# Kernel tuning notes

Hardware: AMD Instinct MI355X
Metric: run time of the kernel (lower is better)

Reference implementation:

```python
import jax, jax.numpy as jnp
import numpy as np

D_MODEL = 1024
NUM_HEADS = 16
DEPTH = D_MODEL // NUM_HEADS


def setup_inputs() -> dict:
    key = jax.random.key(0)
    ks = jax.random.split(key, 9)
    B, S = 2, 2048
    s = 1.0 / np.sqrt(D_MODEL)
    return {
        "x": jax.random.normal(ks[0], (B, S, D_MODEL), dtype=jnp.float32),
        "wq": jax.random.normal(ks[1], (D_MODEL, D_MODEL), dtype=jnp.float32) * s,
        "bq": jnp.zeros((D_MODEL,), dtype=jnp.float32),
        "wk": jax.random.normal(ks[2], (D_MODEL, D_MODEL), dtype=jnp.float32) * s,
        "bk": jnp.zeros((D_MODEL,), dtype=jnp.float32),
        "wv": jax.random.normal(ks[3], (D_MODEL, D_MODEL), dtype=jnp.float32) * s,
        "bv": jnp.zeros((D_MODEL,), dtype=jnp.float32),
        "wo": jax.random.normal(ks[4], (D_MODEL, D_MODEL), dtype=jnp.float32) * s,
        "bo": jnp.zeros((D_MODEL,), dtype=jnp.float32),
    }


def _split_heads(t):
    # [B, S, D] -> [B, H, S, depth]
    B, S, _ = t.shape
    return t.reshape(B, S, NUM_HEADS, DEPTH).transpose(0, 2, 1, 3)


def reference(x, wq, bq, wk, bk, wv, bv, wo, bo):
    B, S, _ = x.shape
    q = _split_heads(x @ wq + bq)
    k = _split_heads(x @ wk + bk)
    v = _split_heads(x @ wv + bv)
    scale = 1.0 / jnp.sqrt(jnp.asarray(DEPTH, dtype=x.dtype))
    logits = jnp.einsum("bhsd,bhtd->bhst", q, k) * scale  # [B,H,S,S]
    attn = jax.nn.softmax(logits, axis=-1)
    ctx = jnp.einsum("bhst,bhtd->bhsd", attn, v)  # [B,H,S,depth]
    concat = ctx.transpose(0, 2, 1, 3).reshape(B, S, D_MODEL)
    return concat @ wo + bo
```

## Files before the change

### kernel.cpp

```cpp
#include <hip/hip_runtime.h>
#include <hip/hip_bf16.h>

typedef __bf16 bf16;
typedef __bf16 bf16x4 __attribute__((ext_vector_type(4)));
typedef __bf16 bf16x8 __attribute__((ext_vector_type(8)));
typedef float f32x4 __attribute__((ext_vector_type(4)));

typedef __attribute__((address_space(3))) void lds_void;
typedef const __attribute__((address_space(1))) void gbl_void;

#define D_MODEL 1024
#define NHEAD 16
#define DEPTH 64
#define SEQ 2048
#define BATCH 2
#define NTOK (BATCH * SEQ)

#define Q_SCALE 0.18033688f

__global__ __launch_bounds__(256) void prep(const float* __restrict__ w0,
                                            const float* __restrict__ w1,
                                            const float* __restrict__ w2,
                                            const float* __restrict__ w3,
                                            const float* __restrict__ x,
                                            bf16* __restrict__ wtb,
                                            bf16* __restrict__ xb) {
    int z = blockIdx.z;
    int tx = threadIdx.x, ty = threadIdx.y;
    if (z < 4) {
        const float* w = (z == 0) ? w0 : (z == 1) ? w1 : (z == 2) ? w2 : w3;
        bf16* d = wtb + (size_t)z * D_MODEL * D_MODEL;
        __shared__ float tile[32][33];
        int c0 = blockIdx.x * 32;
        int r0 = blockIdx.y * 32;
#pragma unroll
        for (int i = 0; i < 4; i++)
            tile[ty + i * 8][tx] = w[(size_t)(r0 + ty + i * 8) * D_MODEL + c0 + tx];
        __syncthreads();
#pragma unroll
        for (int i = 0; i < 4; i++)
            d[(size_t)(c0 + ty + i * 8) * D_MODEL + r0 + tx] = (bf16)tile[tx][ty + i * 8];
    } else {
        int t = ty * 32 + tx;
        size_t i = ((size_t)(z - 4) * 1024 + blockIdx.y * 32 + blockIdx.x) * 256 + t;
        float4 v = ((const float4*)x)[i];
        bf16x4 o = {(bf16)v.x, (bf16)v.y, (bf16)v.z, (bf16)v.w};
        *(bf16x4*)&xb[i * 4] = o;
    }
}

__global__ __launch_bounds__(512, 2) void qkv_gemm(const bf16* __restrict__ xb,
                                                   const bf16* __restrict__ wtb,
                                                   const float* __restrict__ bq,
                                                   const float* __restrict__ bk,
                                                   const float* __restrict__ bv,
                                                   bf16* __restrict__ q,
                                                   bf16* __restrict__ k,
                                                   bf16* __restrict__ v) {
    __shared__ bf16 sm[65536];

    const int flat = blockIdx.x;
    const int wg = (flat & 7) * 24 + (flat >> 3);
    const int mt = wg & 15, nt = wg >> 4;
    const int row0 = mt << 8;
    const int z = nt >> 2;
    const int nb = (nt & 3) << 8;

    const int tid = threadIdx.x;
    const int lane = tid & 63, wave = tid >> 6;
    const int wm = wave >> 2, wn = wave & 3;
    const int quad = lane >> 4, l16 = lane & 15;
    const int kch = ((quad ^ ((l16 >> 1) & 3)) << 3);

    const int srow = lane >> 2;
    const int scg = (lane & 3) ^ ((lane >> 3) & 3);
    const int stDst = wave * 1024 + lane * 8;

    const bf16* Ag = xb + (size_t)(row0 + wave * 32 + srow) * D_MODEL + scg * 8;
    const bf16* Bg = wtb + (size_t)z * D_MODEL * D_MODEL
                   + (size_t)(nb + wave * 32 + srow) * D_MODEL + scg * 8;

    f32x4 acc[8][4] = {};
    bf16x8 bfr[4];

#define GLL(SRC, DST) __builtin_amdgcn_global_load_lds((gbl_void*)(SRC), (lds_void*)(DST), 16, 0, 0)
#define STG_A(T_, KQ_, BUF_) { \
    const bf16* s_ = Ag + (T_) * 64 + (KQ_) * 32; \
    bf16* d_ = sm + (BUF_) * 16384 + (KQ_) * 8192 + stDst; \
    GLL(s_, d_); GLL(s_ + 16 * D_MODEL, d_ + 512); }
#define STG_B(T_, KQ_, BUF_) { \
    const bf16* s_ = Bg + (T_) * 64 + (KQ_) * 32; \
    bf16* d_ = sm + 32768 + (BUF_) * 16384 + (KQ_) * 8192 + stDst; \
    GLL(s_, d_); GLL(s_ + 16 * D_MODEL, d_ + 512); }
#define WAIT6 { asm volatile("s_waitcnt vmcnt(6)" ::: "memory"); }
#define NOW

#define PHASE(BUF_, KQ_, MQ_, STG_STMT, WAIT_STMT) { \
    bf16x8 af[4]; \
    const int ab_ = (BUF_) * 16384 + (KQ_) * 8192 + (wm * 128 + (MQ_) * 64 + l16) * 32 + kch; \
    _Pragma("unroll") \
    for (int i_ = 0; i_ < 4; i_++) af[i_] = *(const bf16x8*)&sm[ab_ + i_ * 512]; \
    if ((MQ_) == 0) { \
        const int bb_ = 32768 + (BUF_) * 16384 + (KQ_) * 8192 + (wn * 64 + l16) * 32 + kch; \
        _Pragma("unroll") \
        for (int j_ = 0; j_ < 4; j_++) bfr[j_] = *(const bf16x8*)&sm[bb_ + j_ * 512]; \
    } \
    STG_STMT; \
    WAIT_STMT; \
    __builtin_amdgcn_sched_barrier(0); \
    __builtin_amdgcn_s_barrier(); \
    __builtin_amdgcn_s_setprio(1); \
    _Pragma("unroll") \
    for (int i_ = 0; i_ < 4; i_++) \
        _Pragma("unroll") \
        for (int j_ = 0; j_ < 4; j_++) \
            acc[(MQ_) * 4 + i_][j_] = __builtin_amdgcn_mfma_f32_16x16x32_bf16( \
                af[i_], bfr[j_], acc[(MQ_) * 4 + i_][j_], 0, 0, 0); \
    __builtin_amdgcn_s_setprio(0); \
    __builtin_amdgcn_sched_barrier(0); \
    __builtin_amdgcn_s_barrier(); }

    STG_B(0, 0, 0);
    STG_A(0, 0, 0);
    STG_B(0, 1, 0);
    STG_A(0, 1, 0);
    asm volatile("s_waitcnt vmcnt(4)" ::: "memory");
    STG_B(1, 0, 1);
    STG_A(1, 0, 1);
    STG_B(1, 1, 1);
    asm volatile("s_waitcnt vmcnt(6)" ::: "memory");
    __builtin_amdgcn_sched_barrier(0);
    __builtin_amdgcn_s_barrier();

#pragma unroll 1
    for (int it = 0; it < 8; ++it) {
        const int t1 = 2 * it + 1;
        const int t2 = (2 * it + 2) & 15;
        const int t3 = (2 * it + 3) & 15;
        PHASE(0, 0, 0, STG_A(t1, 1, 1), NOW)
        PHASE(0, 0, 1, STG_B(t2, 0, 0), NOW)
        PHASE(0, 1, 0, STG_A(t2, 0, 0), NOW)
        PHASE(0, 1, 1, STG_B(t2, 1, 0), WAIT6)
        PHASE(1, 0, 0, STG_A(t2, 1, 0), NOW)
        PHASE(1, 0, 1, STG_B(t3, 0, 1), NOW)
        PHASE(1, 1, 0, STG_A(t3, 0, 1), NOW)
        PHASE(1, 1, 1, STG_B(t3, 1, 1), WAIT6)
    }

#undef PHASE
#undef WAIT6
#undef NOW
#undef STG_A
#undef STG_B
#undef GLL

    const float* bias = (z == 0) ? bq : (z == 1) ? bk : bv;
    const int bI = row0 >> 11;
    const int sBase = row0 & 2047;
    if (z < 2) {
        bf16* dst = (z == 0) ? q : k;
        const float scl = (z == 0) ? Q_SCALE : 1.0f;
#pragma unroll
        for (int j = 0; j < 4; j++) {
            const int f = nb + wn * 64 + j * 16 + l16;
            const float bi = bias[f];
            const int hh = f >> 6, d = f & 63;
            bf16* dcol = dst + ((size_t)(bI * NHEAD + hh) * SEQ) * DEPTH + d;
#pragma unroll
            for (int mi = 0; mi < 8; mi++) {
                const int s0 = sBase + wm * 128 + (mi >> 2) * 64 + (mi & 3) * 16 + quad * 4;
#pragma unroll
                for (int r = 0; r < 4; r++)
                    dcol[(size_t)(s0 + r) * DEPTH] = (bf16)((acc[mi][j][r] + bi) * scl);
            }
        }
    } else {
#pragma unroll
        for (int j = 0; j < 4; j++) {
            const int f = nb + wn * 64 + j * 16 + l16;
            const float bi = bias[f];
            const int hh = f >> 6, d = f & 63;
            bf16* vrow = v + ((size_t)(bI * NHEAD + hh) * DEPTH + d) * SEQ;
#pragma unroll
            for (int mi = 0; mi < 8; mi++) {
                const int s0 = sBase + wm * 128 + (mi >> 2) * 64 + (mi & 3) * 16 + quad * 4;
                f32x4 a = acc[mi][j];
                bf16x4 ob = {(bf16)(a[0] + bi), (bf16)(a[1] + bi),
                             (bf16)(a[2] + bi), (bf16)(a[3] + bi)};
                *(bf16x4*)&vrow[s0] = ob;
            }
        }
    }
}

__global__ __launch_bounds__(256) void attn(const bf16* __restrict__ q,
                                            const bf16* __restrict__ k,
                                            const bf16* __restrict__ v,
                                            bf16* __restrict__ ctx) {
    __shared__ bf16 Ks[64 * 64];
    __shared__ bf16 Vs[64 * 64];
    __shared__ bf16 Ps[4][16 * 64];
    const int tid = threadIdx.x;
    const int lane = tid & 63, wave = tid >> 6;
    const int quad = lane >> 4, l16 = lane & 15;
    const int m7 = l16 & 7;
    const int bh = blockIdx.x;
    const int q0 = blockIdx.y * 64;
    const size_t hb = (size_t)bh * SEQ * DEPTH;
    const bf16* qh = q + hb;
    const bf16* kh = k + hb;
    const bf16* vh = v + hb;

    bf16x8 bq_[2];
    {
        int qrow = q0 + wave * 16 + l16;
#pragma unroll
        for (int c = 0; c < 2; c++)
            bq_[c] = *(const bf16x8*)&qh[(size_t)qrow * DEPTH + c * 32 + quad * 8];
    }
    bf16* myP = &Ps[wave][0];

    bf16x8 ones;
#pragma unroll
    for (int i = 0; i < 8; i++) ones[i] = (bf16)1.0f;

    f32x4 ov[4] = {};
    f32x4 lacc = {};

    const int srow = tid >> 2, ch0 = (tid & 3) * 2, sm7 = srow & 7;
    const bf16* kg = kh + (size_t)srow * DEPTH + ch0 * 8;
    const bf16* vg = vh + (size_t)srow * SEQ + ch0 * 8;
    bf16* ksd0 = &Ks[srow * 64 + ((ch0)     ^ sm7) * 8];
    bf16* ksd1 = &Ks[srow * 64 + ((ch0 + 1) ^ sm7) * 8];
    bf16* vsd0 = &Vs[srow * 64 + ((ch0)     ^ sm7) * 8];
    bf16* vsd1 = &Vs[srow * 64 + ((ch0 + 1) ^ sm7) * 8];

    bf16x8 kr0 = *(const bf16x8*)kg, kr1 = *(const bf16x8*)(kg + 8);
    bf16x8 vr0 = *(const bf16x8*)vg, vr1 = *(const bf16x8*)(vg + 8);

    for (int t0 = 0; t0 < SEQ; t0 += 64) {
        __syncthreads();
        *(bf16x8*)ksd0 = kr0;  *(bf16x8*)ksd1 = kr1;
        *(bf16x8*)vsd0 = vr0;  *(bf16x8*)vsd1 = vr1;
        __syncthreads();
        if (t0 + 64 < SEQ) {
            const bf16* kgn = kg + (size_t)(t0 + 64) * DEPTH;
            const bf16* vgn = vg + (t0 + 64);
            kr0 = *(const bf16x8*)kgn;  kr1 = *(const bf16x8*)(kgn + 8);
            vr0 = *(const bf16x8*)vgn;  vr1 = *(const bf16x8*)(vgn + 8);
        }
        f32x4 sc[4] = {};
#pragma unroll
        for (int c = 0; c < 2; c++)
#pragma unroll
            for (int j = 0; j < 4; j++) {
                bf16x8 kf = *(const bf16x8*)&Ks[(j * 16 + l16) * 64 +
                                                ((((c << 2) | quad) ^ m7) << 3)];
                sc[j] = __builtin_amdgcn_mfma_f32_16x16x32_bf16(kf, bq_[c], sc[j], 0, 0, 0);
            }
#pragma unroll
        for (int j = 0; j < 4; j++) {
            bf16x4 pb = {(bf16)__builtin_amdgcn_exp2f(sc[j][0]),
                         (bf16)__builtin_amdgcn_exp2f(sc[j][1]),
                         (bf16)__builtin_amdgcn_exp2f(sc[j][2]),
                         (bf16)__builtin_amdgcn_exp2f(sc[j][3])};
            int pos = (2 * j + (quad >> 1)) ^ m7;
            *(bf16x4*)&myP[l16 * 64 + pos * 8 + (quad & 1) * 4] = pb;
        }
#pragma unroll
        for (int c = 0; c < 2; c++) {
            bf16x8 pf = *(const bf16x8*)&myP[l16 * 64 + ((((c << 2) | quad) ^ m7) << 3)];
            lacc = __builtin_amdgcn_mfma_f32_16x16x32_bf16(ones, pf, lacc, 0, 0, 0);
#pragma unroll
            for (int t = 0; t < 4; t++) {
                bf16x8 vf = *(const bf16x8*)&Vs[(t * 16 + l16) * 64 +
                                                ((((c << 2) | quad) ^ m7) << 3)];
                ov[t] = __builtin_amdgcn_mfma_f32_16x16x32_bf16(vf, pf, ov[t], 0, 0, 0);
            }
        }
    }
    int b = bh >> 4, hh = bh & 15;
    float inv = 1.0f / lacc[0];
    size_t rowb = ((size_t)(b * SEQ + q0 + wave * 16 + l16)) * D_MODEL + hh * 64;
#pragma unroll
    for (int t = 0; t < 4; t++) {
        bf16x4 ob = {(bf16)(ov[t][0] * inv), (bf16)(ov[t][1] * inv),
                     (bf16)(ov[t][2] * inv), (bf16)(ov[t][3] * inv)};
        *(bf16x4*)&ctx[rowb + t * 16 + quad * 4] = ob;
    }
}

__global__ __launch_bounds__(256) void out_gemm(const bf16* __restrict__ ctx,
                                                const bf16* __restrict__ wot,
                                                const float* __restrict__ bo,
                                                float* __restrict__ out) {
    __shared__ bf16 As[64 * 32];
    __shared__ bf16 Bs[128 * 32];
    const int tid = threadIdx.x;
    const int lane = tid & 63, wave = tid >> 6;
    const int quad = lane >> 4, l16 = lane & 15;
    const int srow = lane >> 2, selem = (lane & 3) * 8;
    int row0 = blockIdx.y * 64, col0 = blockIdx.x * 128;
    f32x4 acc[4][2] = {};

    for (int k0 = 0; k0 < D_MODEL; k0 += 32) {
        __syncthreads();
        {
            const bf16* ga = ctx + (size_t)(row0 + wave * 16 + srow) * D_MODEL + k0 + selem;
            __builtin_amdgcn_global_load_lds((gbl_void*)ga, (lds_void*)(As + wave * 512 + lane * 8), 16, 0, 0);
        }
#pragma unroll
        for (int t = 0; t < 2; t++) {
            int m = wave * 2 + t;
            const bf16* gb = wot + (size_t)(col0 + m * 16 + srow) * D_MODEL + k0 + selem;
            __builtin_amdgcn_global_load_lds((gbl_void*)gb, (lds_void*)(Bs + m * 512 + lane * 8), 16, 0, 0);
        }
        __syncthreads();
        bf16x8 af[4], bfr[2];
#pragma unroll
        for (int i = 0; i < 4; i++)
            af[i] = *(const bf16x8*)&As[(i * 16 + l16) * 32 + quad * 8];
#pragma unroll
        for (int j = 0; j < 2; j++)
            bfr[j] = *(const bf16x8*)&Bs[(wave * 32 + j * 16 + l16) * 32 + quad * 8];
#pragma unroll
        for (int i = 0; i < 4; i++)
#pragma unroll
            for (int j = 0; j < 2; j++)
                acc[i][j] = __builtin_amdgcn_mfma_f32_16x16x32_bf16(af[i], bfr[j], acc[i][j], 0, 0, 0);
    }
#pragma unroll
    for (int i = 0; i < 4; i++)
#pragma unroll
        for (int j = 0; j < 2; j++) {
            int colg = col0 + wave * 32 + j * 16 + l16;
            float bi = bo[colg];
            int rbase = row0 + i * 16 + quad * 4;
#pragma unroll
            for (int r = 0; r < 4; r++)
                out[(size_t)(rbase + r) * D_MODEL + colg] = acc[i][j][r] + bi;
        }
}

extern "C" void kernel_launch(void* const* d_in, const int* in_sizes, int n_in,
                              void* d_out, int out_size, void* d_ws, size_t ws_size,
                              hipStream_t stream) {
    const float* x  = (const float*)d_in[0];
    const float* wq = (const float*)d_in[1];
    const float* bq = (const float*)d_in[2];
    const float* wk = (const float*)d_in[3];
    const float* bk = (const float*)d_in[4];
    const float* wv = (const float*)d_in[5];
    const float* bv = (const float*)d_in[6];
    const float* wo = (const float*)d_in[7];
    const float* bo = (const float*)d_in[8];
    float* out = (float*)d_out;

    const size_t MB = 1024 * 1024;
    char* ws = (char*)d_ws;
    bf16* xb  = (bf16*)(ws);
    bf16* wtb = (bf16*)(ws + 8 * MB);
    bf16* qb  = (bf16*)(ws + 16 * MB);
    bf16* kb  = (bf16*)(ws + 24 * MB);
    bf16* vb  = (bf16*)(ws + 32 * MB);
    bf16* ctx = (bf16*)(ws + 40 * MB);

    prep<<<dim3(32, 32, 8), dim3(32, 8), 0, stream>>>(wq, wk, wv, wo, x, wtb, xb);
    qkv_gemm<<<dim3(192), dim3(512), 0, stream>>>(xb, wtb, bq, bk, bv, qb, kb, vb);
    attn<<<dim3(BATCH * NHEAD, SEQ / 64), 256, 0, stream>>>(qb, kb, vb, ctx);
    out_gemm<<<dim3(8, 64), 256, 0, stream>>>(ctx, wtb + 3 * (size_t)D_MODEL * D_MODEL, bo, out);
}
```

Before: 194.7 us.

## Split attention keys across waves, load K/V straight to registers, reduce via LDS

The attention kernel no longer stages K/V tiles in shared memory behind block-wide barriers. Each wave now handles all 64 query rows of the block but only its own slice of the key sequence. K and V fragments are read directly from global memory into registers, with K double-buffered across unrolled steps. Row sums are accumulated in scalar registers instead of a ones-vector MFMA. Partial outputs and sums from the four waves are combined through a shared-memory reduction at the end. This removes per-tile __syncthreads and LDS traffic, at the cost of more registers (16 accumulator tiles), uncoalesced global fragment loads, and a final reduction.

```diff
diff --git a/kernel.cpp b/kernel.cpp
--- a/kernel.cpp
+++ b/kernel.cpp
@@ -193,17 +193,14 @@
     }
 }
 
-__global__ __launch_bounds__(256) void attn(const bf16* __restrict__ q,
-                                            const bf16* __restrict__ k,
-                                            const bf16* __restrict__ v,
-                                            bf16* __restrict__ ctx) {
-    __shared__ bf16 Ks[64 * 64];
-    __shared__ bf16 Vs[64 * 64];
-    __shared__ bf16 Ps[4][16 * 64];
+__global__ __launch_bounds__(256, 2) void attn(const bf16* __restrict__ q,
+                                               const bf16* __restrict__ k,
+                                               const bf16* __restrict__ v,
+                                               bf16* __restrict__ ctx) {
+    __shared__ f32x4 red[4][17][64];
     const int tid = threadIdx.x;
     const int lane = tid & 63, wave = tid >> 6;
     const int quad = lane >> 4, l16 = lane & 15;
-    const int m7 = l16 & 7;
     const int bh = blockIdx.x;
     const int q0 = blockIdx.y * 64;
     const size_t hb = (size_t)bh * SEQ * DEPTH;
@@ -211,82 +208,105 @@
     const bf16* kh = k + hb;
     const bf16* vh = v + hb;
 
-    bf16x8 bq_[2];
-    {
-        int qrow = q0 + wave * 16 + l16;
+    bf16x8 bq_[4][2];
+#pragma unroll
+    for (int n = 0; n < 4; n++) {
+        int qrow = q0 + n * 16 + l16;
 #pragma unroll
         for (int c = 0; c < 2; c++)
-            bq_[c] = *(const bf16x8*)&qh[(size_t)qrow * DEPTH + c * 32 + quad * 8];
-    }
-    bf16* myP = &Ps[wave][0];
-
-    bf16x8 ones;
-#pragma unroll
-    for (int i = 0; i < 8; i++) ones[i] = (bf16)1.0f;
-
-    f32x4 ov[4] = {};
-    f32x4 lacc = {};
-
-    const int srow = tid >> 2, ch0 = (tid & 3) * 2, sm7 = srow & 7;
-    const bf16* kg = kh + (size_t)srow * DEPTH + ch0 * 8;
-    const bf16* vg = vh + (size_t)srow * SEQ + ch0 * 8;
-    bf16* ksd0 = &Ks[srow * 64 + ((ch0)     ^ sm7) * 8];
-    bf16* ksd1 = &Ks[srow * 64 + ((ch0 + 1) ^ sm7) * 8];
-    bf16* vsd0 = &Vs[srow * 64 + ((ch0)     ^ sm7) * 8];
-    bf16* vsd1 = &Vs[srow * 64 + ((ch0 + 1) ^ sm7) * 8];
-
-    bf16x8 kr0 = *(const bf16x8*)kg, kr1 = *(const bf16x8*)(kg + 8);
-    bf16x8 vr0 = *(const bf16x8*)vg, vr1 = *(const bf16x8*)(vg + 8);
-
-    for (int t0 = 0; t0 < SEQ; t0 += 64) {
-        __syncthreads();
-        *(bf16x8*)ksd0 = kr0;  *(bf16x8*)ksd1 = kr1;
-        *(bf16x8*)vsd0 = vr0;  *(bf16x8*)vsd1 = vr1;
-        __syncthreads();
-        if (t0 + 64 < SEQ) {
-            const bf16* kgn = kg + (size_t)(t0 + 64) * DEPTH;
-            const bf16* vgn = vg + (t0 + 64);
-            kr0 = *(const bf16x8*)kgn;  kr1 = *(const bf16x8*)(kgn + 8);
-            vr0 = *(const bf16x8*)vgn;  vr1 = *(const bf16x8*)(vgn + 8);
-        }
-        f32x4 sc[4] = {};
-#pragma unroll
-        for (int c = 0; c < 2; c++)
-#pragma unroll
-            for (int j = 0; j < 4; j++) {
-                bf16x8 kf = *(const bf16x8*)&Ks[(j * 16 + l16) * 64 +
-                                                ((((c << 2) | quad) ^ m7) << 3)];
-                sc[j] = __builtin_amdgcn_mfma_f32_16x16x32_bf16(kf, bq_[c], sc[j], 0, 0, 0);
-            }
-#pragma unroll
-        for (int j = 0; j < 4; j++) {
-            bf16x4 pb = {(bf16)__builtin_amdgcn_exp2f(sc[j][0]),
-                         (bf16)__builtin_amdgcn_exp2f(sc[j][1]),
-                         (bf16)__builtin_amdgcn_exp2f(sc[j][2]),
-                         (bf16)__builtin_amdgcn_exp2f(sc[j][3])};
-            int pos = (2 * j + (quad >> 1)) ^ m7;
-            *(bf16x4*)&myP[l16 * 64 + pos * 8 + (quad & 1) * 4] = pb;
-        }
-#pragma unroll
-        for (int c = 0; c < 2; c++) {
-            bf16x8 pf = *(const bf16x8*)&myP[l16 * 64 + ((((c << 2) | quad) ^ m7) << 3)];
-            lacc = __builtin_amdgcn_mfma_f32_16x16x32_bf16(ones, pf, lacc, 0, 0, 0);
-#pragma unroll
-            for (int t = 0; t < 4; t++) {
-                bf16x8 vf = *(const bf16x8*)&Vs[(t * 16 + l16) * 64 +
-                                                ((((c << 2) | quad) ^ m7) << 3)];
-                ov[t] = __builtin_amdgcn_mfma_f32_16x16x32_bf16(vf, pf, ov[t], 0, 0, 0);
-            }
-        }
-    }
-    int b = bh >> 4, hh = bh & 15;
-    float inv = 1.0f / lacc[0];
-    size_t rowb = ((size_t)(b * SEQ + q0 + wave * 16 + l16)) * D_MODEL + hh * 64;
-#pragma unroll
-    for (int t = 0; t < 4; t++) {
-        bf16x4 ob = {(bf16)(ov[t][0] * inv), (bf16)(ov[t][1] * inv),
-                     (bf16)(ov[t][2] * inv), (bf16)(ov[t][3] * inv)};
-        *(bf16x4*)&ctx[rowb + t * 16 + quad * 4] = ob;
+            bq_[n][c] = *(const bf16x8*)&qh[(size_t)qrow * DEPTH + c * 32 + quad * 8];
+    }
+
+    const int klane = (wave * 32 + (l16 >> 2) * 8 + (l16 & 3)) * DEPTH + quad * 8;
+    const int vlane = l16 * SEQ + wave * 32 + quad * 8;
+
+    f32x4 ov[4][4] = {};
+    float lsum[4] = {0.f, 0.f, 0.f, 0.f};
+
+    bf16x8 ka[2][2], kb2[2][2];
+
+#define LOADK(KF, T_) { \
+    const bf16* kp_ = kh + (size_t)(T_) * DEPTH + klane; \
+    KF[0][0] = *(const bf16x8*)(kp_); \
+    KF[0][1] = *(const bf16x8*)(kp_ + 32); \
+    KF[1][0] = *(const bf16x8*)(kp_ + 256); \
+    KF[1][1] = *(const bf16x8*)(kp_ + 288); }
+
+#define COMPUTE(KF, T_) { \
+    bf16x8 vf[4]; \
+    _Pragma("unroll") \
+    for (int t_ = 0; t_ < 4; t_++) \
+        vf[t_] = *(const bf16x8*)(vh + (size_t)t_ * 16 * SEQ + vlane + (T_)); \
+    f32x4 s0[4] = {}, s1[4] = {}; \
+    _Pragma("unroll") \
+    for (int n_ = 0; n_ < 4; n_++) { \
+        s0[n_] = __builtin_amdgcn_mfma_f32_16x16x32_bf16(KF[0][0], bq_[n_][0], s0[n_], 0, 0, 0); \
+        s0[n_] = __builtin_amdgcn_mfma_f32_16x16x32_bf16(KF[0][1], bq_[n_][1], s0[n_], 0, 0, 0); \
+        s1[n_] = __builtin_amdgcn_mfma_f32_16x16x32_bf16(KF[1][0], bq_[n_][0], s1[n_], 0, 0, 0); \
+        s1[n_] = __builtin_amdgcn_mfma_f32_16x16x32_bf16(KF[1][1], bq_[n_][1], s1[n_], 0, 0, 0); \
+    } \
+    bf16x8 pb[4]; \
+    _Pragma("unroll") \
+    for (int n_ = 0; n_ < 4; n_++) { \
+        float e0a = __builtin_amdgcn_exp2f(s0[n_][0]); \
+        float e0b = __builtin_amdgcn_exp2f(s0[n_][1]); \
+        float e0c = __builtin_amdgcn_exp2f(s0[n_][2]); \
+        float e0d = __builtin_amdgcn_exp2f(s0[n_][3]); \
+        float e1a = __builtin_amdgcn_exp2f(s1[n_][0]); \
+        float e1b = __builtin_amdgcn_exp2f(s1[n_][1]); \
+        float e1c = __builtin_amdgcn_exp2f(s1[n_][2]); \
+        float e1d = __builtin_amdgcn_exp2f(s1[n_][3]); \
+        pb[n_][0] = (bf16)e0a; pb[n_][1] = (bf16)e0b; \
+        pb[n_][2] = (bf16)e0c; pb[n_][3] = (bf16)e0d; \
+        pb[n_][4] = (bf16)e1a; pb[n_][5] = (bf16)e1b; \
+        pb[n_][6] = (bf16)e1c; pb[n_][7] = (bf16)e1d; \
+        lsum[n_] += ((e0a + e0b) + (e0c + e0d)) + ((e1a + e1b) + (e1c + e1d)); \
+    } \
+    _Pragma("unroll") \
+    for (int t_ = 0; t_ < 4; t_++) \
+        _Pragma("unroll") \
+        for (int n_ = 0; n_ < 4; n_++) \
+            ov[t_][n_] = __builtin_amdgcn_mfma_f32_16x16x32_bf16(vf[t_], pb[n_], ov[t_][n_], 0, 0, 0); }
+
+    LOADK(ka, 0);
+#pragma unroll 1
+    for (int t0 = 0; t0 < SEQ; t0 += 256) {
+        LOADK(kb2, t0 + 128);
+        COMPUTE(ka, t0);
+        LOADK(ka, (t0 + 256) & (SEQ - 1));
+        COMPUTE(kb2, t0 + 128);
+    }
+#undef COMPUTE
+#undef LOADK
+
+#pragma unroll
+    for (int t = 0; t < 4; t++)
+#pragma unroll
+        for (int n = 0; n < 4; n++)
+            red[wave][t * 4 + n][lane] = ov[t][n];
+    f32x4 lv = {lsum[0], lsum[1], lsum[2], lsum[3]};
+    red[wave][16][lane] = lv;
+    __syncthreads();
+
+    f32x4 ls = {};
+#pragma unroll
+    for (int w_ = 0; w_ < 4; w_++)
+#pragma unroll
+        for (int q_ = 0; q_ < 4; q_++)
+            ls += red[w_][16][l16 + q_ * 16];
+    f32x4 inv4 = {1.0f / ls[0], 1.0f / ls[1], 1.0f / ls[2], 1.0f / ls[3]};
+
+    const int b = bh >> 4, hh = bh & 15;
+#pragma unroll
+    for (int n = 0; n < 4; n++) {
+        f32x4 s = red[0][wave * 4 + n][lane] + red[1][wave * 4 + n][lane]
+                + red[2][wave * 4 + n][lane] + red[3][wave * 4 + n][lane];
+        float iv = inv4[n];
+        bf16x4 ob = {(bf16)(s[0] * iv), (bf16)(s[1] * iv),
+                     (bf16)(s[2] * iv), (bf16)(s[3] * iv)};
+        size_t off = ((size_t)(b * SEQ + q0 + n * 16 + l16)) * D_MODEL
+                   + hh * 64 + wave * 16 + quad * 4;
+        *(bf16x4*)&ctx[off] = ob;
     }
 }
 
```

Result: slower. 208.6 us (+7.1%).
